# Kernel tuning notes

Measured on AMD Instinct MI355X. Metric: run time of the kernel, lower is better.

## Reference

```python
import jax, jax.numpy as jnp
import numpy as np

N = 100000
E = 1250000
D = 64
POS_DIM = 3


def _linear_params(key, fan_in, fan_out, bias=True):
    k1, k2 = jax.random.split(key)
    bound = 1.0 / np.sqrt(fan_in)
    W = jax.random.uniform(k1, (fan_in, fan_out), minval=-bound, maxval=bound, dtype=jnp.float32)
    if bias:
        b = jax.random.uniform(k2, (fan_out,), minval=-bound, maxval=bound, dtype=jnp.float32)
        return W, b
    return W


def setup_inputs() -> dict:
    key = jax.random.key(0)
    ks = jax.random.split(key, 10)
    x = jax.random.normal(ks[0], (N, D), dtype=jnp.float32)
    pos = jax.random.normal(ks[1], (N, POS_DIM), dtype=jnp.float32)
    edge_index = jax.random.randint(ks[2], (2, E), 0, N, dtype=jnp.int64)
    W_in, b_in = _linear_params(ks[3], D, D)
    W_lin = _linear_params(ks[4], D, D, bias=False)
    W_src = _linear_params(ks[5], D, D, bias=False)
    W_dst = _linear_params(ks[6], D, D, bias=False)
    W_pos, b_pos = _linear_params(ks[7], POS_DIM, D)
    W_out, b_out = _linear_params(ks[8], D, D)
    return {"x": x, "pos": pos, "edge_index": edge_index,
            "W_in": W_in, "b_in": b_in, "W_lin": W_lin, "W_src": W_src,
            "W_dst": W_dst, "W_pos": W_pos, "b_pos": b_pos,
            "W_out": W_out, "b_out": b_out}


def reference(x, pos, edge_index, W_in, b_in, W_lin, W_src, W_dst, W_pos, b_pos, W_out, b_out):
    n = x.shape[0]
    src, dst = edge_index[0], edge_index[1]  # j, i (PyG source_to_target)
    # lin_in + relu
    h = jax.nn.relu(x @ W_in + b_in)  # [N, D]
    # PointTransformerConv projections
    x_lin = h @ W_lin      # value projection, gathered at src (x_j)
    a_src = h @ W_src      # alpha_j side
    a_dst = h @ W_dst      # alpha_i side
    # per-edge positional MLP on pos_i - pos_j
    delta = (pos[dst] - pos[src]) @ W_pos + b_pos  # [E, D]
    # per-edge attention logits, per channel
    alpha = a_dst[dst] - a_src[src] + delta  # [E, D]
    # segment softmax over destination node groups (PyG softmax, eps=1e-16)
    seg_max = jax.ops.segment_max(alpha, dst, num_segments=n)
    alpha = jnp.exp(alpha - seg_max[dst])
    seg_sum = jax.ops.segment_sum(alpha, dst, num_segments=n)
    alpha = alpha / (seg_sum[dst] + 1e-16)
    # weighted messages, scatter-add aggregate
    msg = alpha * (x_lin[src] + delta)  # [E, D]
    out = jax.ops.segment_sum(msg, dst, num_segments=n)  # [N, D]
    # lin_out + relu
    return jax.nn.relu(out @ W_out + b_out)
```

## Files before the change

### kernel.cpp

```cpp
#include <hip/hip_runtime.h>

#define NN 100000
#define NE 1250000
#define NWIN 782
#define GA 256
#define CHUNK ((NE + GA - 1) / GA)
#define CAP16 16
#define OVFCAP 131072
#define WEDCAP 40

typedef __attribute__((ext_vector_type(4))) float f32x4;
typedef __attribute__((ext_vector_type(8))) short s16x8;

__device__ __forceinline__ short bfb(float f) {
    union { float f; unsigned u; } c; c.f = f;
    unsigned u = c.u + 0x7fffu + ((c.u >> 16) & 1u);
    return (short)(u >> 16);
}
__device__ __forceinline__ void splitbf(float v, short& hi, short& lo) {
    hi = bfb(v);
    union { unsigned u; float f; } c; c.u = ((unsigned)(unsigned short)hi) << 16;
    lo = bfb(v - c.f);
}
__device__ __forceinline__ float lo2f(unsigned u) {
    union { unsigned u; float f; } c; c.u = u << 16; return c.f;
}
__device__ __forceinline__ float hi2f(unsigned u) {
    union { unsigned u; float f; } c; c.u = u & 0xffff0000u; return c.f;
}

__global__ __launch_bounds__(256) void k_prep(
    const float* __restrict__ Wi, const float* __restrict__ Wl,
    const float* __restrict__ Ws, const float* __restrict__ Wo,
    short* __restrict__ P, int* __restrict__ ovf_cnt,
    unsigned* __restrict__ AXb)
{
    const int t = blockIdx.x * 256 + threadIdx.x;
    if (t == 0) *ovf_cnt = 0;
    if (t < 64) AXb[(size_t)NN * 64 + t] = 0u;
    if (t >= 2048) return;
    const int mat = t >> 9, rem = t & 511;
    const int lane = rem & 63, cfg = rem >> 6;
    const int kh = cfg >> 2, nt = cfg & 3;
    const int m = lane & 15, q = lane >> 4;
    const float* W = mat == 0 ? Wi : mat == 1 ? Wl : mat == 2 ? Ws : Wo;
    s16x8 v;
    #pragma unroll
    for (int i = 0; i < 8; ++i)
        v[i] = bfb(W[(kh * 32 + q * 8 + i) * 64 + nt * 16 + m]);
    *(s16x8*)&P[(size_t)t * 8] = v;
}

__global__ __launch_bounds__(256) void k_front(
    const int* __restrict__ ei, unsigned* __restrict__ stage, int* __restrict__ gcnt,
    int2* __restrict__ ovf, int* __restrict__ ovf_cnt,
    const float* __restrict__ x, const short* __restrict__ P,
    const float* __restrict__ b_in,
    const float* __restrict__ pos, const float* __restrict__ W_pos,
    unsigned* __restrict__ AXb)
{
    __shared__ int lcnt[NWIN];
    __shared__ float hT[4][16 * 68];

    if (blockIdx.x < GA) {
        const int g = blockIdx.x;
        for (int i = threadIdx.x; i < NWIN; i += 256) lcnt[i] = 0;
        __syncthreads();
        unsigned* myStage = stage + (size_t)g * NWIN * CAP16;
        const int e0 = g * CHUNK;
        const int e1 = (e0 + CHUNK < NE) ? e0 + CHUNK : NE;
        for (int e = e0 + threadIdx.x; e < e1; e += 256) {
            const int s = ei[e], d = ei[NE + e];
            const int b = d >> 7;
            const int c = atomicAdd(&lcnt[b], 1);
            if (c < CAP16) {
                myStage[b * CAP16 + c] = (unsigned)s | ((unsigned)(d & 127) << 17);
            } else {
                const int o = atomicAdd(ovf_cnt, 1);
                if (o < OVFCAP) ovf[o] = make_int2(s, d);
            }
        }
        __syncthreads();
        for (int i = threadIdx.x; i < NWIN; i += 256)
            gcnt[i * GA + g] = lcnt[i] < CAP16 ? lcnt[i] : CAP16;
        return;
    }

    const int lane = threadIdx.x & 63;
    const int wid  = threadIdx.x >> 6;
    const int m = lane & 15, q = lane >> 4;

    s16x8 Wf[3][2][4];
    #pragma unroll
    for (int mat = 0; mat < 3; ++mat)
        #pragma unroll
        for (int kh = 0; kh < 2; ++kh)
            #pragma unroll
            for (int nt = 0; nt < 4; ++nt)
                Wf[mat][kh][nt] = *(const s16x8*)&P[((size_t)mat * 512 + (kh * 4 + nt) * 64 + lane) * 8];
    float bin[4], wpv0[4], wpv1[4], wpv2[4];
    #pragma unroll
    for (int nt = 0; nt < 4; ++nt) {
        bin[nt]  = b_in[nt * 16 + m];
        wpv0[nt] = W_pos[nt * 16 + m];
        wpv1[nt] = W_pos[64 + nt * 16 + m];
        wpv2[nt] = W_pos[128 + nt * 16 + m];
    }

    const int wave = (blockIdx.x - GA) * 4 + wid, nw = (gridDim.x - GA) * 4;
    for (int chunk = wave; chunk < NN / 16; chunk += nw) {
        const int r0 = chunk * 16;
        const float* xr = x + (size_t)(r0 + m) * 64;
        float xv[16];
        *(float4*)&xv[0]  = *(const float4*)(xr + q * 8);
        *(float4*)&xv[4]  = *(const float4*)(xr + q * 8 + 4);
        *(float4*)&xv[8]  = *(const float4*)(xr + 32 + q * 8);
        *(float4*)&xv[12] = *(const float4*)(xr + 32 + q * 8 + 4);
        s16x8 ahi0, alo0, ahi1, alo1;
        #pragma unroll
        for (int i = 0; i < 8; ++i) {
            short h, l;
            splitbf(xv[i], h, l);     ahi0[i] = h; alo0[i] = l;
            splitbf(xv[8 + i], h, l); ahi1[i] = h; alo1[i] = l;
        }
        #pragma unroll
        for (int nt = 0; nt < 4; ++nt) {
            f32x4 acc = {0.f, 0.f, 0.f, 0.f};
            acc = __builtin_amdgcn_mfma_f32_16x16x32_bf16(alo0, Wf[0][0][nt], acc, 0, 0, 0);
            acc = __builtin_amdgcn_mfma_f32_16x16x32_bf16(alo1, Wf[0][1][nt], acc, 0, 0, 0);
            acc = __builtin_amdgcn_mfma_f32_16x16x32_bf16(ahi0, Wf[0][0][nt], acc, 0, 0, 0);
            acc = __builtin_amdgcn_mfma_f32_16x16x32_bf16(ahi1, Wf[0][1][nt], acc, 0, 0, 0);
            #pragma unroll
            for (int r = 0; r < 4; ++r) {
                float hv = acc[r] + bin[nt];
                hT[wid][(q * 4 + r) * 68 + nt * 16 + m] = hv > 0.f ? hv : 0.f;
            }
        }
        float hv[16];
        *(float4*)&hv[0]  = *(const float4*)&hT[wid][m * 68 + q * 8];
        *(float4*)&hv[4]  = *(const float4*)&hT[wid][m * 68 + q * 8 + 4];
        *(float4*)&hv[8]  = *(const float4*)&hT[wid][m * 68 + 32 + q * 8];
        *(float4*)&hv[12] = *(const float4*)&hT[wid][m * 68 + 32 + q * 8 + 4];
        s16x8 hhi0, hlo0, hhi1, hlo1;
        #pragma unroll
        for (int i = 0; i < 8; ++i) {
            short h, l;
            splitbf(hv[i], h, l);     hhi0[i] = h; hlo0[i] = l;
            splitbf(hv[8 + i], h, l); hhi1[i] = h; hlo1[i] = l;
        }
        float px[4], py[4], pz[4];
        #pragma unroll
        for (int r = 0; r < 4; ++r) {
            const float* pp = pos + (size_t)(r0 + q * 4 + r) * 3;
            px[r] = pp[0]; py[r] = pp[1]; pz[r] = pp[2];
        }
        #pragma unroll
        for (int nt = 0; nt < 4; ++nt) {
            f32x4 aS = {0.f, 0.f, 0.f, 0.f}, aL = {0.f, 0.f, 0.f, 0.f};
            aS = __builtin_amdgcn_mfma_f32_16x16x32_bf16(hlo0, Wf[2][0][nt], aS, 0, 0, 0);
            aS = __builtin_amdgcn_mfma_f32_16x16x32_bf16(hlo1, Wf[2][1][nt], aS, 0, 0, 0);
            aS = __builtin_amdgcn_mfma_f32_16x16x32_bf16(hhi0, Wf[2][0][nt], aS, 0, 0, 0);
            aS = __builtin_amdgcn_mfma_f32_16x16x32_bf16(hhi1, Wf[2][1][nt], aS, 0, 0, 0);
            aL = __builtin_amdgcn_mfma_f32_16x16x32_bf16(hlo0, Wf[1][0][nt], aL, 0, 0, 0);
            aL = __builtin_amdgcn_mfma_f32_16x16x32_bf16(hlo1, Wf[1][1][nt], aL, 0, 0, 0);
            aL = __builtin_amdgcn_mfma_f32_16x16x32_bf16(hhi0, Wf[1][0][nt], aL, 0, 0, 0);
            aL = __builtin_amdgcn_mfma_f32_16x16x32_bf16(hhi1, Wf[1][1][nt], aL, 0, 0, 0);
            #pragma unroll
            for (int r = 0; r < 4; ++r) {
                const float sp = fmaf(px[r], wpv0[nt], fmaf(py[r], wpv1[nt], pz[r] * wpv2[nt]));
                const float ev = __expf(-(aS[r] + sp));
                const float ex = ev * (aL[r] - sp);
                const unsigned p = (unsigned)(unsigned short)bfb(ev)
                                 | ((unsigned)(unsigned short)bfb(ex) << 16);
                AXb[(size_t)(r0 + q * 4 + r) * 64 + nt * 16 + m] = p;
            }
        }
    }
}

__global__ __launch_bounds__(256) void k_passB(
    const unsigned* __restrict__ stage, const int* __restrict__ gcnt,
    const int2* __restrict__ ovf, const int* __restrict__ ovf_cnt,
    int* __restrict__ slots, int* __restrict__ deg)
{
    __shared__ int slotsL[128 * WEDCAP];
    __shared__ int cntL[128];
    const int b = blockIdx.x;
    const int t = threadIdx.x;
    if (t < 128) cntL[t] = 0;
    __syncthreads();
    const int n = min(gcnt[b * GA + t], CAP16);
    const unsigned* cell = stage + (size_t)t * NWIN * CAP16 + b * CAP16;
    uint4 q0 = *(const uint4*)cell;
    uint4 q1 = *(const uint4*)(cell + 4);
    uint4 q2 = *(const uint4*)(cell + 8);
    uint4 q3 = *(const uint4*)(cell + 12);
    const unsigned eb[16] = {q0.x, q0.y, q0.z, q0.w, q1.x, q1.y, q1.z, q1.w,
                             q2.x, q2.y, q2.z, q2.w, q3.x, q3.y, q3.z, q3.w};
    #pragma unroll
    for (int i = 0; i < CAP16; ++i)
        if (i < n) {
            const int d7 = (int)(eb[i] >> 17);
            const int c = atomicAdd(&cntL[d7], 1);
            if (c < WEDCAP) slotsL[d7 * WEDCAP + c] = (int)(eb[i] & 0x1ffff);
        }
    const int no = min(*ovf_cnt, OVFCAP);
    for (int i = t; i < no; i += 256) {
        const int2 sd = ovf[i];
        if ((sd.y >> 7) == b) {
            const int d7 = sd.y & 127;
            const int c = atomicAdd(&cntL[d7], 1);
            if (c < WEDCAP) slotsL[d7 * WEDCAP + c] = sd.x;
        }
    }
    __syncthreads();
    int4* dstq = (int4*)(slots + (size_t)b * 128 * WEDCAP);
    const int4* srcq = (const int4*)slotsL;
    #pragma unroll
    for (int i = 0; i < 5; ++i) dstq[i * 256 + t] = srcq[i * 256 + t];
    if (t < 128) {
        const int d = (b << 7) + t;
        if (d < NN) deg[d] = cntL[t] < WEDCAP ? cntL[t] : WEDCAP;
    }
}

__global__ __launch_bounds__(256) void k_agg(
    const int* __restrict__ deg_arr, const int* __restrict__ slots,
    const float* __restrict__ pos,
    const float* __restrict__ W_pos, const float* __restrict__ b_pos,
    const unsigned* __restrict__ AXb, float* __restrict__ V)
{
    const int lane = threadIdx.x & 63;
    const int d = __builtin_amdgcn_readfirstlane((int)((blockIdx.x * 256 + threadIdx.x) >> 6));
    if (d >= NN) return;
    const float pd0 = pos[d * 3 + 0], pd1 = pos[d * 3 + 1], pd2 = pos[d * 3 + 2];
    const float dlb = fmaf(pd0, W_pos[lane],
                      fmaf(pd1, W_pos[64 + lane],
                      fmaf(pd2, W_pos[128 + lane], b_pos[lane])));

    int deg = deg_arr[d]; deg = deg < WEDCAP ? deg : WEDCAP;
    const int* srow = slots + (size_t)d * WEDCAP;

    float Sa = 0.f, Ua = 0.f;
    if (deg > 0) {
        int cs[4], ns[4];
        unsigned cax[4], nax[4];
        {
            const int4 qd = *(const int4*)srow;
            cs[0] = qd.x;
            cs[1] = (1 < deg) ? qd.y : NN;
            cs[2] = (2 < deg) ? qd.z : NN;
            cs[3] = (3 < deg) ? qd.w : NN;
            #pragma unroll
            for (int k = 0; k < 4; ++k)
                cax[k] = AXb[(unsigned)(cs[k] * 64 + lane)];
        }
        for (int j = 0; j < deg; j += 8) {
            if (j + 4 < deg) {
                const int4 qd = *(const int4*)(srow + j + 4);
                ns[0] = qd.x;
                ns[1] = (j + 5 < deg) ? qd.y : NN;
                ns[2] = (j + 6 < deg) ? qd.z : NN;
                ns[3] = (j + 7 < deg) ? qd.w : NN;
                #pragma unroll
                for (int k = 0; k < 4; ++k)
                    nax[k] = AXb[(unsigned)(ns[k] * 64 + lane)];
            }
            #pragma unroll
            for (int k = 0; k < 4; ++k) {
                Sa += lo2f(cax[k]);
                Ua += hi2f(cax[k]);
            }
            if (j + 8 < deg) {
                const int4 qd = *(const int4*)(srow + j + 8);
                cs[0] = qd.x;
                cs[1] = (j + 9  < deg) ? qd.y : NN;
                cs[2] = (j + 10 < deg) ? qd.z : NN;
                cs[3] = (j + 11 < deg) ? qd.w : NN;
                #pragma unroll
                for (int k = 0; k < 4; ++k)
                    cax[k] = AXb[(unsigned)(cs[k] * 64 + lane)];
            }
            if (j + 4 < deg) {
                #pragma unroll
                for (int k = 0; k < 4; ++k) {
                    Sa += lo2f(nax[k]);
                    Ua += hi2f(nax[k]);
                }
            }
        }
    }
    const float v = (deg > 0) ? Ua / (Sa + 1e-16f) + dlb : 0.f;
    V[(size_t)d * 64 + lane] = v;
}

__global__ __launch_bounds__(256) void k_node_out(
    const float* __restrict__ V, const short* __restrict__ P,
    const float* __restrict__ b_out, float* __restrict__ out)
{
    const int lane = threadIdx.x & 63;
    const int wid  = threadIdx.x >> 6;
    const int m = lane & 15, q = lane >> 4;

    s16x8 Wf[2][4];
    #pragma unroll
    for (int kh = 0; kh < 2; ++kh)
        #pragma unroll
        for (int nt = 0; nt < 4; ++nt)
            Wf[kh][nt] = *(const s16x8*)&P[((size_t)3 * 512 + (kh * 4 + nt) * 64 + lane) * 8];
    float bo[4];
    #pragma unroll
    for (int nt = 0; nt < 4; ++nt) bo[nt] = b_out[nt * 16 + m];

    const int wave = blockIdx.x * 4 + wid, nw = gridDim.x * 4;
    for (int chunk = wave; chunk < NN / 16; chunk += nw) {
        const int r0 = chunk * 16;
        const float* vr = V + (size_t)(r0 + m) * 64;
        float vv[16];
        *(float4*)&vv[0]  = *(const float4*)(vr + q * 8);
        *(float4*)&vv[4]  = *(const float4*)(vr + q * 8 + 4);
        *(float4*)&vv[8]  = *(const float4*)(vr + 32 + q * 8);
        *(float4*)&vv[12] = *(const float4*)(vr + 32 + q * 8 + 4);
        s16x8 ahi0, alo0, ahi1, alo1;
        #pragma unroll
        for (int i = 0; i < 8; ++i) {
            short h, l;
            splitbf(vv[i], h, l);     ahi0[i] = h; alo0[i] = l;
            splitbf(vv[8 + i], h, l); ahi1[i] = h; alo1[i] = l;
        }
        #pragma unroll
        for (int nt = 0; nt < 4; ++nt) {
            f32x4 acc = {0.f, 0.f, 0.f, 0.f};
            acc = __builtin_amdgcn_mfma_f32_16x16x32_bf16(alo0, Wf[0][nt], acc, 0, 0, 0);
            acc = __builtin_amdgcn_mfma_f32_16x16x32_bf16(alo1, Wf[1][nt], acc, 0, 0, 0);
            acc = __builtin_amdgcn_mfma_f32_16x16x32_bf16(ahi0, Wf[0][nt], acc, 0, 0, 0);
            acc = __builtin_amdgcn_mfma_f32_16x16x32_bf16(ahi1, Wf[1][nt], acc, 0, 0, 0);
            #pragma unroll
            for (int r = 0; r < 4; ++r) {
                float o = acc[r] + bo[nt];
                out[(size_t)(r0 + q * 4 + r) * 64 + nt * 16 + m] = o > 0.f ? o : 0.f;
            }
        }
    }
}

extern "C" void kernel_launch(void* const* d_in, const int* in_sizes, int n_in,
                              void* d_out, int out_size, void* d_ws, size_t ws_size,
                              hipStream_t stream) {
    const float* x     = (const float*)d_in[0];
    const float* pos   = (const float*)d_in[1];
    const int*   ei    = (const int*)d_in[2];
    const float* W_in  = (const float*)d_in[3];
    const float* b_in  = (const float*)d_in[4];
    const float* W_lin = (const float*)d_in[5];
    const float* W_src = (const float*)d_in[6];
    const float* W_pos = (const float*)d_in[8];
    const float* b_pos = (const float*)d_in[9];
    const float* W_out = (const float*)d_in[10];
    const float* b_out = (const float*)d_in[11];

    unsigned* AXb   = (unsigned*)d_ws;
    unsigned* stage = AXb + (size_t)(NN + 1) * 64;
    int*      gcnt  = (int*)(stage + (size_t)GA * NWIN * CAP16);
    int*      slots = gcnt + (size_t)NWIN * GA;
    int*      deg   = slots + (size_t)NWIN * 128 * WEDCAP;
    float*    V     = (float*)(deg + NN);
    int2*     ovf   = (int2*)(V + (size_t)NN * 64);
    int*      ovfc  = (int*)(ovf + OVFCAP);
    short*    P     = (short*)(ovfc + 64);

    k_prep    <<<8,        256, 0, stream>>>(W_in, W_lin, W_src, W_out, P, ovfc, AXb);
    k_front   <<<GA + 512, 256, 0, stream>>>(ei, stage, gcnt, ovf, ovfc,
                                             x, P, b_in, pos, W_pos, AXb);
    k_passB   <<<NWIN,     256, 0, stream>>>(stage, gcnt, ovf, ovfc, slots, deg);
    k_agg     <<<(NN + 3) / 4, 256, 0, stream>>>(deg, slots, pos, W_pos, b_pos, AXb, V);
    k_node_out<<<512,      256, 0, stream>>>(V, P, b_out, (float*)d_out);
}
```

Measured before the change: 186.9 us.

## Fuse per-node aggregation with output linear layer via shared-memory staging

Merges the aggregation kernel and the output-projection kernel into one. Each wave aggregates 16 destination nodes in sequence, writes their 64-channel results into a padded shared-memory tile, then runs the bf16-split MFMA output linear layer and ReLU directly from that tile. This removes the global round trip of the N×64 intermediate V and one kernel launch. In exchange, each wave handles 16 nodes serially, so there are far fewer waves in flight to hide gather latency.

Measured after the change: 184.0 us. About the same (-1.6%).

```diff
diff --git a/kernel.cpp b/kernel.cpp
--- a/kernel.cpp
+++ b/kernel.cpp
@@ -224,83 +224,84 @@
     }
 }
 
-__global__ __launch_bounds__(256) void k_agg(
+__global__ __launch_bounds__(256) void k_agg_out(
     const int* __restrict__ deg_arr, const int* __restrict__ slots,
     const float* __restrict__ pos,
     const float* __restrict__ W_pos, const float* __restrict__ b_pos,
-    const unsigned* __restrict__ AXb, float* __restrict__ V)
-{
-    const int lane = threadIdx.x & 63;
-    const int d = __builtin_amdgcn_readfirstlane((int)((blockIdx.x * 256 + threadIdx.x) >> 6));
-    if (d >= NN) return;
-    const float pd0 = pos[d * 3 + 0], pd1 = pos[d * 3 + 1], pd2 = pos[d * 3 + 2];
-    const float dlb = fmaf(pd0, W_pos[lane],
-                      fmaf(pd1, W_pos[64 + lane],
-                      fmaf(pd2, W_pos[128 + lane], b_pos[lane])));
-
-    int deg = deg_arr[d]; deg = deg < WEDCAP ? deg : WEDCAP;
-    const int* srow = slots + (size_t)d * WEDCAP;
-
-    float Sa = 0.f, Ua = 0.f;
-    if (deg > 0) {
-        int cs[4], ns[4];
-        unsigned cax[4], nax[4];
-        {
-            const int4 qd = *(const int4*)srow;
-            cs[0] = qd.x;
-            cs[1] = (1 < deg) ? qd.y : NN;
-            cs[2] = (2 < deg) ? qd.z : NN;
-            cs[3] = (3 < deg) ? qd.w : NN;
-            #pragma unroll
-            for (int k = 0; k < 4; ++k)
-                cax[k] = AXb[(unsigned)(cs[k] * 64 + lane)];
-        }
-        for (int j = 0; j < deg; j += 8) {
-            if (j + 4 < deg) {
-                const int4 qd = *(const int4*)(srow + j + 4);
-                ns[0] = qd.x;
-                ns[1] = (j + 5 < deg) ? qd.y : NN;
-                ns[2] = (j + 6 < deg) ? qd.z : NN;
-                ns[3] = (j + 7 < deg) ? qd.w : NN;
-                #pragma unroll
-                for (int k = 0; k < 4; ++k)
-                    nax[k] = AXb[(unsigned)(ns[k] * 64 + lane)];
-            }
-            #pragma unroll
-            for (int k = 0; k < 4; ++k) {
-                Sa += lo2f(cax[k]);
-                Ua += hi2f(cax[k]);
-            }
-            if (j + 8 < deg) {
-                const int4 qd = *(const int4*)(srow + j + 8);
-                cs[0] = qd.x;
-                cs[1] = (j + 9  < deg) ? qd.y : NN;
-                cs[2] = (j + 10 < deg) ? qd.z : NN;
-                cs[3] = (j + 11 < deg) ? qd.w : NN;
-                #pragma unroll
-                for (int k = 0; k < 4; ++k)
-                    cax[k] = AXb[(unsigned)(cs[k] * 64 + lane)];
-            }
-            if (j + 4 < deg) {
-                #pragma unroll
-                for (int k = 0; k < 4; ++k) {
-                    Sa += lo2f(nax[k]);
-                    Ua += hi2f(nax[k]);
-                }
-            }
-        }
-    }
-    const float v = (deg > 0) ? Ua / (Sa + 1e-16f) + dlb : 0.f;
-    V[(size_t)d * 64 + lane] = v;
-}
-
-__global__ __launch_bounds__(256) void k_node_out(
-    const float* __restrict__ V, const short* __restrict__ P,
+    const unsigned* __restrict__ AXb, const short* __restrict__ P,
     const float* __restrict__ b_out, float* __restrict__ out)
 {
+    __shared__ float vT[4][16 * 68];
     const int lane = threadIdx.x & 63;
     const int wid  = threadIdx.x >> 6;
     const int m = lane & 15, q = lane >> 4;
+    const int base = __builtin_amdgcn_readfirstlane(blockIdx.x * 64 + wid * 16);
+    if (base >= NN) return;
+
+    const float wp0 = W_pos[lane], wp1 = W_pos[64 + lane],
+                wp2 = W_pos[128 + lane], bp = b_pos[lane];
+
+    for (int t = 0; t < 16; ++t) {
+        const int d = base + t;
+        float v = 0.f;
+        if (d < NN) {
+            const float pd0 = pos[d * 3 + 0], pd1 = pos[d * 3 + 1], pd2 = pos[d * 3 + 2];
+            const float dlb = fmaf(pd0, wp0, fmaf(pd1, wp1, fmaf(pd2, wp2, bp)));
+            int deg = deg_arr[d]; deg = deg < WEDCAP ? deg : WEDCAP;
+            const int* srow = slots + (size_t)d * WEDCAP;
+            float Sa = 0.f, Ua = 0.f;
+            if (deg > 0) {
+                int cs[4], ns[4];
+                unsigned cax[4], nax[4];
+                {
+                    const int4 qd = *(const int4*)srow;
+                    cs[0] = qd.x;
+                    cs[1] = (1 < deg) ? qd.y : NN;
+                    cs[2] = (2 < deg) ? qd.z : NN;
+                    cs[3] = (3 < deg) ? qd.w : NN;
+                    #pragma unroll
+                    for (int k = 0; k < 4; ++k)
+                        cax[k] = AXb[(unsigned)(cs[k] * 64 + lane)];
+                }
+                for (int j = 0; j < deg; j += 8) {
+                    if (j + 4 < deg) {
+                        const int4 qd = *(const int4*)(srow + j + 4);
+                        ns[0] = qd.x;
+                        ns[1] = (j + 5 < deg) ? qd.y : NN;
+                        ns[2] = (j + 6 < deg) ? qd.z : NN;
+                        ns[3] = (j + 7 < deg) ? qd.w : NN;
+                        #pragma unroll
+                        for (int k = 0; k < 4; ++k)
+                            nax[k] = AXb[(unsigned)(ns[k] * 64 + lane)];
+                    }
+                    #pragma unroll
+                    for (int k = 0; k < 4; ++k) {
+                        Sa += lo2f(cax[k]);
+                        Ua += hi2f(cax[k]);
+                    }
+                    if (j + 8 < deg) {
+                        const int4 qd = *(const int4*)(srow + j + 8);
+                        cs[0] = qd.x;
+                        cs[1] = (j + 9  < deg) ? qd.y : NN;
+                        cs[2] = (j + 10 < deg) ? qd.z : NN;
+                        cs[3] = (j + 11 < deg) ? qd.w : NN;
+                        #pragma unroll
+                        for (int k = 0; k < 4; ++k)
+                            cax[k] = AXb[(unsigned)(cs[k] * 64 + lane)];
+                    }
+                    if (j + 4 < deg) {
+                        #pragma unroll
+                        for (int k = 0; k < 4; ++k) {
+                            Sa += lo2f(nax[k]);
+                            Ua += hi2f(nax[k]);
+                        }
+                    }
+                }
+                v = Ua / (Sa + 1e-16f) + dlb;
+            }
+        }
+        vT[wid][t * 68 + lane] = v;
+    }
 
     s16x8 Wf[2][4];
     #pragma unroll
@@ -312,33 +313,31 @@
     #pragma unroll
     for (int nt = 0; nt < 4; ++nt) bo[nt] = b_out[nt * 16 + m];
 
-    const int wave = blockIdx.x * 4 + wid, nw = gridDim.x * 4;
-    for (int chunk = wave; chunk < NN / 16; chunk += nw) {
-        const int r0 = chunk * 16;
-        const float* vr = V + (size_t)(r0 + m) * 64;
-        float vv[16];
-        *(float4*)&vv[0]  = *(const float4*)(vr + q * 8);
-        *(float4*)&vv[4]  = *(const float4*)(vr + q * 8 + 4);
-        *(float4*)&vv[8]  = *(const float4*)(vr + 32 + q * 8);
-        *(float4*)&vv[12] = *(const float4*)(vr + 32 + q * 8 + 4);
-        s16x8 ahi0, alo0, ahi1, alo1;
-        #pragma unroll
-        for (int i = 0; i < 8; ++i) {
-            short h, l;
-            splitbf(vv[i], h, l);     ahi0[i] = h; alo0[i] = l;
-            splitbf(vv[8 + i], h, l); ahi1[i] = h; alo1[i] = l;
-        }
-        #pragma unroll
-        for (int nt = 0; nt < 4; ++nt) {
-            f32x4 acc = {0.f, 0.f, 0.f, 0.f};
-            acc = __builtin_amdgcn_mfma_f32_16x16x32_bf16(alo0, Wf[0][nt], acc, 0, 0, 0);
-            acc = __builtin_amdgcn_mfma_f32_16x16x32_bf16(alo1, Wf[1][nt], acc, 0, 0, 0);
-            acc = __builtin_amdgcn_mfma_f32_16x16x32_bf16(ahi0, Wf[0][nt], acc, 0, 0, 0);
-            acc = __builtin_amdgcn_mfma_f32_16x16x32_bf16(ahi1, Wf[1][nt], acc, 0, 0, 0);
-            #pragma unroll
-            for (int r = 0; r < 4; ++r) {
+    float vv[16];
+    *(float4*)&vv[0]  = *(const float4*)&vT[wid][m * 68 + q * 8];
+    *(float4*)&vv[4]  = *(const float4*)&vT[wid][m * 68 + q * 8 + 4];
+    *(float4*)&vv[8]  = *(const float4*)&vT[wid][m * 68 + 32 + q * 8];
+    *(float4*)&vv[12] = *(const float4*)&vT[wid][m * 68 + 32 + q * 8 + 4];
+    s16x8 ahi0, alo0, ahi1, alo1;
+    #pragma unroll
+    for (int i = 0; i < 8; ++i) {
+        short h, l;
+        splitbf(vv[i], h, l);     ahi0[i] = h; alo0[i] = l;
+        splitbf(vv[8 + i], h, l); ahi1[i] = h; alo1[i] = l;
+    }
+    #pragma unroll
+    for (int nt = 0; nt < 4; ++nt) {
+        f32x4 acc = {0.f, 0.f, 0.f, 0.f};
+        acc = __builtin_amdgcn_mfma_f32_16x16x32_bf16(alo0, Wf[0][nt], acc, 0, 0, 0);
+        acc = __builtin_amdgcn_mfma_f32_16x16x32_bf16(alo1, Wf[1][nt], acc, 0, 0, 0);
+        acc = __builtin_amdgcn_mfma_f32_16x16x32_bf16(ahi0, Wf[0][nt], acc, 0, 0, 0);
+        acc = __builtin_amdgcn_mfma_f32_16x16x32_bf16(ahi1, Wf[1][nt], acc, 0, 0, 0);
+        #pragma unroll
+        for (int r = 0; r < 4; ++r) {
+            const int row = base + q * 4 + r;
+            if (row < NN) {
                 float o = acc[r] + bo[nt];
-                out[(size_t)(r0 + q * 4 + r) * 64 + nt * 16 + m] = o > 0.f ? o : 0.f;
+                out[(size_t)row * 64 + nt * 16 + m] = o > 0.f ? o : 0.f;
             }
         }
     }
@@ -364,15 +363,14 @@
     int*      gcnt  = (int*)(stage + (size_t)GA * NWIN * CAP16);
     int*      slots = gcnt + (size_t)NWIN * GA;
     int*      deg   = slots + (size_t)NWIN * 128 * WEDCAP;
-    float*    V     = (float*)(deg + NN);
-    int2*     ovf   = (int2*)(V + (size_t)NN * 64);
+    int2*     ovf   = (int2*)(deg + NN);
     int*      ovfc  = (int*)(ovf + OVFCAP);
     short*    P     = (short*)(ovfc + 64);
 
-    k_prep    <<<8,        256, 0, stream>>>(W_in, W_lin, W_src, W_out, P, ovfc, AXb);
-    k_front   <<<GA + 512, 256, 0, stream>>>(ei, stage, gcnt, ovf, ovfc,
-                                             x, P, b_in, pos, W_pos, AXb);
-    k_passB   <<<NWIN,     256, 0, stream>>>(stage, gcnt, ovf, ovfc, slots, deg);
-    k_agg     <<<(NN + 3) / 4, 256, 0, stream>>>(deg, slots, pos, W_pos, b_pos, AXb, V);
-    k_node_out<<<512,      256, 0, stream>>>(V, P, b_out, (float*)d_out);
-}
+    k_prep   <<<8,        256, 0, stream>>>(W_in, W_lin, W_src, W_out, P, ovfc, AXb);
+    k_front  <<<GA + 512, 256, 0, stream>>>(ei, stage, gcnt, ovf, ovfc,
+                                            x, P, b_in, pos, W_pos, AXb);
+    k_passB  <<<NWIN,     256, 0, stream>>>(stage, gcnt, ovf, ovfc, slots, deg);
+    k_agg_out<<<(NN + 63) / 64, 256, 0, stream>>>(deg, slots, pos, W_pos, b_pos,
+                                                  AXb, P, b_out, (float*)d_out);
+}
```
